# Optimization experiments

Measured on AMD Instinct MI355X. Metric: run time of the kernel, lower is better.

## Reference

```python
import jax, jax.numpy as jnp
import numpy as np

B, N, C = 4, 2048, 768
H = 12
D = C // H  # 64
HID = 4 * C  # 3072
EPS = 1e-5


def layer_norm(x, g, b):
    mu = jnp.mean(x, axis=-1, keepdims=True)
    var = jnp.mean(jnp.square(x - mu), axis=-1, keepdims=True)
    return (x - mu) * jax.lax.rsqrt(var + EPS) * g + b


def setup_inputs() -> dict:
    key = jax.random.key(0)
    ks = jax.random.split(key, 12)
    s = lambda fan_in: 1.0 / np.sqrt(fan_in)
    return {
        "x": jax.random.normal(ks[0], (B, N, C), jnp.float32),
        "ln1_g": jnp.ones((C,), jnp.float32),
        "ln1_b": jnp.zeros((C,), jnp.float32),
        "qkv_w": jax.random.normal(ks[1], (3 * C, C), jnp.float32) * s(C),
        "proj_w": jax.random.normal(ks[2], (C, C), jnp.float32) * s(C),
        "proj_b": jnp.zeros((C,), jnp.float32),
        "ln2_g": jnp.ones((C,), jnp.float32),
        "ln2_b": jnp.zeros((C,), jnp.float32),
        "fc1_w": jax.random.normal(ks[3], (HID, C), jnp.float32) * s(C),
        "fc1_b": jnp.zeros((HID,), jnp.float32),
        "fc2_w": jax.random.normal(ks[4], (C, HID), jnp.float32) * s(HID),
        "fc2_b": jnp.zeros((C,), jnp.float32),
    }


def reference(x, ln1_g, ln1_b, qkv_w, proj_w, proj_b, ln2_g, ln2_b, fc1_w, fc1_b, fc2_w, fc2_b):
    # ---- attention branch ----
    h = layer_norm(x, ln1_g, ln1_b)
    qkv = jnp.einsum('bnc,fc->bnf', h, qkv_w)            # [B,N,3C]
    qkv = qkv.reshape(B, N, 3, H, D)
    q, k, v = jnp.moveaxis(qkv, 2, 0)                     # each [B,N,H,D]
    q = jnp.transpose(q, (0, 2, 1, 3)) * (D ** -0.5)      # [B,H,N,D]
    k = jnp.transpose(k, (0, 2, 1, 3))
    v = jnp.transpose(v, (0, 2, 1, 3))
    attn = jax.nn.softmax(jnp.einsum('bhnd,bhmd->bhnm', q, k), axis=-1)
    o = jnp.einsum('bhnm,bhmd->bhnd', attn, v)            # [B,H,N,D]
    o = jnp.transpose(o, (0, 2, 1, 3)).reshape(B, N, C)
    o = jnp.einsum('bnc,oc->bno', o, proj_w) + proj_b
    x = x + o
    # ---- MLP branch ----
    h = layer_norm(x, ln2_g, ln2_b)
    h = jnp.einsum('bnc,hc->bnh', h, fc1_w) + fc1_b
    h = jax.nn.gelu(h, approximate=False)
    h = jnp.einsum('bnh,ch->bnc', h, fc2_w) + fc2_b
    return x + h
```

## Files before the change

kernel.cpp:

```cpp
#include <hip/hip_runtime.h>
#include <math.h>

typedef __bf16 bf16;
typedef __bf16 bf16x4 __attribute__((ext_vector_type(4)));
typedef __bf16 bf16x8 __attribute__((ext_vector_type(8)));
typedef float  f32x4  __attribute__((ext_vector_type(4)));

#define B_   4
#define N_   2048
#define C_   768
#define H_   12
#define T_   8192
#define HID_ 3072

typedef const __attribute__((address_space(1))) unsigned int* as1_u32;
typedef __attribute__((address_space(3))) unsigned int* as3_u32;
__device__ __forceinline__ void gl_lds16(const void* g, void* l) {
    __builtin_amdgcn_global_load_lds((as1_u32)g, (as3_u32)l, 16, 0, 0);
}

__global__ __launch_bounds__(256)
void ln_kernel(const float* __restrict__ inp, const float* __restrict__ g,
               const float* __restrict__ bsh, bf16* __restrict__ out)
{
    int wave = threadIdx.x >> 6, lane = threadIdx.x & 63;
    long long row = (long long)blockIdx.x * 4 + wave;
    const float* p = inp + row * C_;
    float v[12];
    #pragma unroll
    for (int i = 0; i < 12; i++) v[i] = p[i * 64 + lane];
    float s = 0.f, s2 = 0.f;
    #pragma unroll
    for (int i = 0; i < 12; i++) { s += v[i]; s2 += v[i] * v[i]; }
    #pragma unroll
    for (int m = 1; m < 64; m <<= 1) {
        s  += __shfl_xor(s,  m, 64);
        s2 += __shfl_xor(s2, m, 64);
    }
    float mu  = s  * (1.f / C_);
    float var = s2 * (1.f / C_) - mu * mu;
    float rs  = rsqrtf(var + 1e-5f);
    bf16* o = out + row * C_;
    #pragma unroll
    for (int i = 0; i < 12; i++) {
        int c = i * 64 + lane;
        o[c] = (bf16)(((v[i] - mu) * rs) * g[c] + bsh[c]);
    }
}

template<int MODE>
__global__ __launch_bounds__(256)
void gemm_bt(const bf16* __restrict__ A, const float* __restrict__ Bw,
             int M, int N, int K,
             const float* __restrict__ bias,
             const float* resid_f,
             void* out, bf16* out2)
{
    __shared__ bf16 At[128 * 32];
    __shared__ bf16 Bt[128 * 32];
    int tid  = threadIdx.x;
    int lane = tid & 63, wave = tid >> 6;
    int quad = lane >> 4, l15 = lane & 15;
    int bm = blockIdx.x, bn = blockIdx.y;
    int wm = wave >> 1, wn = wave & 1;

    f32x4 acc[4][4];
    f32x4 zero = {0.f, 0.f, 0.f, 0.f};
    #pragma unroll
    for (int mt = 0; mt < 4; mt++)
        #pragma unroll
        for (int nt = 0; nt < 4; nt++) acc[mt][nt] = zero;

    int arow = tid >> 2;
    int akof = (tid & 3) << 3;
    const bf16*  ag = A  + (size_t)(bm * 128 + arow) * K + akof;
    const float* bg = Bw + (size_t)(bn * 128 + arow) * K + akof;

    for (int k0 = 0; k0 < K; k0 += 32) {
        gl_lds16(ag,                    &At[tid * 8]);
        gl_lds16(ag + (size_t)64 * K,   &At[2048 + tid * 8]);
        f32x4 b0a = *(const f32x4*)(bg);
        f32x4 b0b = *(const f32x4*)(bg + 4);
        f32x4 b1a = *(const f32x4*)(bg + (size_t)64 * K);
        f32x4 b1b = *(const f32x4*)(bg + (size_t)64 * K + 4);
        bf16x8 b0, b1;
        #pragma unroll
        for (int j = 0; j < 4; j++) {
            b0[j] = (bf16)b0a[j]; b0[4 + j] = (bf16)b0b[j];
            b1[j] = (bf16)b1a[j]; b1[4 + j] = (bf16)b1b[j];
        }
        *(bf16x8*)(&Bt[tid * 8])        = b0;
        *(bf16x8*)(&Bt[2048 + tid * 8]) = b1;
        ag += 32; bg += 32;
        __syncthreads();

        bf16x8 af[4], bfr[4];
        #pragma unroll
        for (int mt = 0; mt < 4; mt++)
            af[mt] = *(const bf16x8*)(&At[(wm * 64 + mt * 16 + l15) * 32 + quad * 8]);
        #pragma unroll
        for (int nt = 0; nt < 4; nt++)
            bfr[nt] = *(const bf16x8*)(&Bt[(wn * 64 + nt * 16 + l15) * 32 + quad * 8]);
        #pragma unroll
        for (int mt = 0; mt < 4; mt++)
            #pragma unroll
            for (int nt = 0; nt < 4; nt++)
                acc[mt][nt] = __builtin_amdgcn_mfma_f32_16x16x32_bf16(
                    af[mt], bfr[nt], acc[mt][nt], 0, 0, 0);
        __syncthreads();
    }

    if (MODE == 3) {
        if (bn < 12) {
            #pragma unroll
            for (int nt = 0; nt < 4; nt++) {
                int col = bn * 128 + wn * 64 + nt * 16 + l15;
                #pragma unroll
                for (int mt = 0; mt < 4; mt++)
                    #pragma unroll
                    for (int r = 0; r < 4; r++) {
                        int row = bm * 128 + wm * 64 + mt * 16 + quad * 4 + r;
                        ((bf16*)out)[(size_t)row * 1536 + col] = (bf16)acc[mt][nt][r];
                    }
            }
        } else {
            int b = bm >> 4;
            #pragma unroll
            for (int nt = 0; nt < 4; nt++) {
                int vcol = bn * 128 - 1536 + wn * 64 + nt * 16 + l15;
                int h = vcol >> 6, d = vcol & 63;
                size_t rowbase = ((size_t)(b * H_ + h) * 64 + d) * N_;
                #pragma unroll
                for (int mt = 0; mt < 4; mt++) {
                    int n0 = (bm & 15) * 128 + wm * 64 + mt * 16 + quad * 4;
                    bf16x4 pv;
                    #pragma unroll
                    for (int r = 0; r < 4; r++) pv[r] = (bf16)acc[mt][nt][r];
                    *(bf16x4*)(&out2[rowbase + n0]) = pv;
                }
            }
        }
    } else {
        #pragma unroll
        for (int nt = 0; nt < 4; nt++) {
            int col = bn * 128 + wn * 64 + nt * 16 + l15;
            float bv = bias[col];
            #pragma unroll
            for (int mt = 0; mt < 4; mt++) {
                #pragma unroll
                for (int r = 0; r < 4; r++) {
                    int row = bm * 128 + wm * 64 + mt * 16 + quad * 4 + r;
                    size_t idx = (size_t)row * N + col;
                    float v = acc[mt][nt][r] + bv;
                    if (MODE == 1) {
                        ((float*)out)[idx] = v + resid_f[idx];
                    } else {
                        float ge = 0.5f * v * (1.f + erff(v * 0.70710678118f));
                        ((bf16*)out)[idx] = (bf16)ge;
                    }
                }
            }
        }
    }
}

__global__ __launch_bounds__(256)
void attn_kernel(const bf16* __restrict__ qk, const bf16* __restrict__ vt,
                 bf16* __restrict__ o)
{
    __shared__ bf16 Kt[2][64 * 64];
    __shared__ bf16 Vt[2][64 * 64];
    __shared__ bf16 Pt[4][2][16 * 64];

    int tid = threadIdx.x, lane = tid & 63, wave = tid >> 6;
    int quad = lane >> 4, l15 = lane & 15;
    int swz = (l15 & 7);
    int blk = blockIdx.x;
    int qb = blk & 15;
    int bh = blk >> 4;
    int b = bh / H_, h = bh % H_;

    const bf16* qbase = qk + (size_t)(b * N_) * 1536 + h * 64;
    const bf16* kbase = qbase + 768;
    const bf16* vtb   = vt + (size_t)(bh * 64) * N_;

    bf16x8 qf[2][2];
    #pragma unroll
    for (int qi = 0; qi < 2; qi++) {
        int q = qb * 128 + wave * 32 + qi * 16 + l15;
        const bf16* qp = qbase + (size_t)q * 1536 + quad * 8;
        qf[qi][0] = *(const bf16x8*)(qp);
        qf[qi][1] = *(const bf16x8*)(qp + 32);
    }

    int srow = tid >> 3, schk = tid & 7;
    int soA = srow * 64 + ((schk ^ (srow & 7)) << 3);
    int soB = (srow + 32) * 64 + ((schk ^ (srow & 7)) << 3);

    bf16x8 kr0, kr1, vr0, vr1;
    const bf16* kg0 = kbase + (size_t)srow * 1536 + schk * 8;
    const bf16* vg0 = vtb + (size_t)srow * N_ + schk * 8;

    {
        kr0 = *(const bf16x8*)(kg0);
        kr1 = *(const bf16x8*)(kg0 + (size_t)32 * 1536);
        vr0 = *(const bf16x8*)(vg0);
        vr1 = *(const bf16x8*)(vg0 + (size_t)32 * N_);
        *(bf16x8*)(&Kt[0][soA]) = kr0;  *(bf16x8*)(&Kt[0][soB]) = kr1;
        *(bf16x8*)(&Vt[0][soA]) = vr0;  *(bf16x8*)(&Vt[0][soB]) = vr1;
    }
    __syncthreads();

    f32x4 oacc[2][4];
    f32x4 zero = {0.f, 0.f, 0.f, 0.f};
    #pragma unroll
    for (int qi = 0; qi < 2; qi++)
        #pragma unroll
        for (int nt = 0; nt < 4; nt++) oacc[qi][nt] = zero;
    float mrun[2] = {-1e30f, -1e30f}, lrun[2] = {0.f, 0.f};

    for (int kt = 0; kt < 32; kt++) {
        int cur = kt & 1;
        if (kt < 31) {
            const bf16* kg = kg0 + (size_t)(kt + 1) * 64 * 1536;
            const bf16* vg = vg0 + (size_t)(kt + 1) * 64;
            kr0 = *(const bf16x8*)(kg);
            kr1 = *(const bf16x8*)(kg + (size_t)32 * 1536);
            vr0 = *(const bf16x8*)(vg);
            vr1 = *(const bf16x8*)(vg + (size_t)32 * N_);
        }
        const bf16* KtC = &Kt[cur][0];
        const bf16* VtC = &Vt[cur][0];

        #pragma unroll
        for (int qi = 0; qi < 2; qi++) {
            f32x4 s[4];
            #pragma unroll
            for (int nt = 0; nt < 4; nt++) {
                const bf16* krow = KtC + (nt * 16 + l15) * 64;
                bf16x8 ka0 = *(const bf16x8*)(krow + ((quad ^ swz) << 3));
                bf16x8 ka1 = *(const bf16x8*)(krow + (((4 + quad) ^ swz) << 3));
                f32x4 sv = zero;
                sv = __builtin_amdgcn_mfma_f32_16x16x32_bf16(ka0, qf[qi][0], sv, 0, 0, 0);
                sv = __builtin_amdgcn_mfma_f32_16x16x32_bf16(ka1, qf[qi][1], sv, 0, 0, 0);
                s[nt] = sv;
            }
            float mx = -1e30f;
            #pragma unroll
            for (int nt = 0; nt < 4; nt++)
                #pragma unroll
                for (int r = 0; r < 4; r++) mx = fmaxf(mx, s[nt][r]);
            mx = fmaxf(mx, __shfl_xor(mx, 16, 64));
            mx = fmaxf(mx, __shfl_xor(mx, 32, 64));
            float mnew = fmaxf(mrun[qi], mx * 0.125f);
            float al   = __expf(mrun[qi] - mnew);
            mrun[qi] = mnew;
            float ps = 0.f;
            #pragma unroll
            for (int nt = 0; nt < 4; nt++)
                #pragma unroll
                for (int r = 0; r < 4; r++) {
                    float pv = __expf(s[nt][r] * 0.125f - mnew);
                    s[nt][r] = pv;
                    ps += pv;
                }
            ps += __shfl_xor(ps, 16, 64);
            ps += __shfl_xor(ps, 32, 64);
            lrun[qi] = lrun[qi] * al + ps;
            #pragma unroll
            for (int nt = 0; nt < 4; nt++) oacc[qi][nt] *= al;
            bf16* pw = &Pt[wave][qi][0];
            #pragma unroll
            for (int nt = 0; nt < 4; nt++) {
                bf16x4 pk;
                #pragma unroll
                for (int r = 0; r < 4; r++) pk[r] = (bf16)s[nt][r];
                int ofs = l15 * 64 + (((nt * 2 + (quad >> 1)) ^ swz) << 3) + ((quad & 1) << 2);
                *(bf16x4*)(&pw[ofs]) = pk;
            }
        }

        #pragma unroll
        for (int kc = 0; kc < 2; kc++) {
            int pofs = l15 * 64 + (((kc * 4 + quad) ^ swz) << 3);
            bf16x8 pb0 = *(const bf16x8*)(&Pt[wave][0][pofs]);
            bf16x8 pb1 = *(const bf16x8*)(&Pt[wave][1][pofs]);
            #pragma unroll
            for (int nt = 0; nt < 4; nt++) {
                bf16x8 va = *(const bf16x8*)(VtC + (nt * 16 + l15) * 64 +
                                             (((kc * 4 + quad) ^ swz) << 3));
                oacc[0][nt] = __builtin_amdgcn_mfma_f32_16x16x32_bf16(va, pb0, oacc[0][nt], 0, 0, 0);
                oacc[1][nt] = __builtin_amdgcn_mfma_f32_16x16x32_bf16(va, pb1, oacc[1][nt], 0, 0, 0);
            }
        }

        if (kt < 31) {
            int nxt = cur ^ 1;
            *(bf16x8*)(&Kt[nxt][soA]) = kr0;  *(bf16x8*)(&Kt[nxt][soB]) = kr1;
            *(bf16x8*)(&Vt[nxt][soA]) = vr0;  *(bf16x8*)(&Vt[nxt][soB]) = vr1;
        }
        __syncthreads();
    }

    #pragma unroll
    for (int qi = 0; qi < 2; qi++) {
        int q = qb * 128 + wave * 32 + qi * 16 + l15;
        float inv = 1.f / lrun[qi];
        bf16* ob = o + (size_t)(b * N_ + q) * C_ + h * 64 + quad * 4;
        #pragma unroll
        for (int nt = 0; nt < 4; nt++) {
            bf16x4 pk;
            #pragma unroll
            for (int r = 0; r < 4; r++) pk[r] = (bf16)(oacc[qi][nt][r] * inv);
            *(bf16x4*)(&ob[nt * 16]) = pk;
        }
    }
}

extern "C" void kernel_launch(void* const* d_in, const int* in_sizes, int n_in,
                              void* d_out, int out_size, void* d_ws, size_t ws_size,
                              hipStream_t stream)
{
    const float* x      = (const float*)d_in[0];
    const float* ln1_g  = (const float*)d_in[1];
    const float* ln1_b  = (const float*)d_in[2];
    const float* qkv_w  = (const float*)d_in[3];
    const float* proj_w = (const float*)d_in[4];
    const float* proj_b = (const float*)d_in[5];
    const float* ln2_g  = (const float*)d_in[6];
    const float* ln2_b  = (const float*)d_in[7];
    const float* fc1_w  = (const float*)d_in[8];
    const float* fc1_b  = (const float*)d_in[9];
    const float* fc2_w  = (const float*)d_in[10];
    const float* fc2_b  = (const float*)d_in[11];
    float* out = (float*)d_out;

    char* ws = (char*)d_ws;
    bf16* QK = (bf16*)ws;
    bf16* VT = (bf16*)(ws + (size_t)T_ * 1536 * 2);
    bf16* G  = (bf16*)ws;
    bf16* R1 = (bf16*)(ws + (size_t)T_ * HID_ * 2);

    ln_kernel<<<T_ / 4, 256, 0, stream>>>(x, ln1_g, ln1_b, R1);
    gemm_bt<3><<<dim3(T_ / 128, 2304 / 128), 256, 0, stream>>>(
        R1, qkv_w, T_, 2304, C_, nullptr, nullptr, QK, VT);
    attn_kernel<<<48 * 16, 256, 0, stream>>>(QK, VT, R1);
    gemm_bt<1><<<dim3(T_ / 128, C_ / 128), 256, 0, stream>>>(
        R1, proj_w, T_, C_, C_, proj_b, x, out, nullptr);
    ln_kernel<<<T_ / 4, 256, 0, stream>>>(out, ln2_g, ln2_b, R1);
    gemm_bt<2><<<dim3(T_ / 128, HID_ / 128), 256, 0, stream>>>(
        R1, fc1_w, T_, HID_, C_, fc1_b, nullptr, G, nullptr);
    gemm_bt<1><<<dim3(T_ / 128, C_ / 128), 256, 0, stream>>>(
        G, fc2_w, T_, C_, HID_, fc2_b, out, out, nullptr);
}
```

Measured before the change: 555.2 us.

## Add swizzled LDS layout and double-buffered 128x64 GEMM for C-output projections

Applies an XOR swizzle to the LDS tile layout in the main GEMM to reduce bank conflicts on fragment reads. Adds a new gemm64 kernel with 128x64 tiles and double-buffered LDS for the proj and fc2 GEMMs (N=768). This doubles the block count on those narrow-output GEMMs for better CU occupancy and overlaps global loads with MFMA. The cost is reloading the A tiles more often, and the B tile is still converted from fp32 synchronously inside the loop.

```diff
diff --git a/kernel.cpp b/kernel.cpp
--- a/kernel.cpp
+++ b/kernel.cpp
@@ -53,7 +53,6 @@
 void gemm_bt(const bf16* __restrict__ A, const float* __restrict__ Bw,
              int M, int N, int K,
              const float* __restrict__ bias,
-             const float* resid_f,
              void* out, bf16* out2)
 {
     __shared__ bf16 At[128 * 32];
@@ -63,6 +62,7 @@
     int quad = lane >> 4, l15 = lane & 15;
     int bm = blockIdx.x, bn = blockIdx.y;
     int wm = wave >> 1, wn = wave & 1;
+    int swz = (l15 >> 1) & 3;
 
     f32x4 acc[4][4];
     f32x4 zero = {0.f, 0.f, 0.f, 0.f};
@@ -72,9 +72,9 @@
         for (int nt = 0; nt < 4; nt++) acc[mt][nt] = zero;
 
     int arow = tid >> 2;
-    int akof = (tid & 3) << 3;
-    const bf16*  ag = A  + (size_t)(bm * 128 + arow) * K + akof;
-    const float* bg = Bw + (size_t)(bn * 128 + arow) * K + akof;
+    int aq   = (tid & 3) ^ ((arow >> 1) & 3);
+    const bf16*  ag = A  + (size_t)(bm * 128 + arow) * K + aq * 8;
+    const float* bg = Bw + (size_t)(bn * 128 + arow) * K + aq * 8;
 
     for (int k0 = 0; k0 < K; k0 += 32) {
         gl_lds16(ag,                    &At[tid * 8]);
@@ -97,10 +97,10 @@
         bf16x8 af[4], bfr[4];
         #pragma unroll
         for (int mt = 0; mt < 4; mt++)
-            af[mt] = *(const bf16x8*)(&At[(wm * 64 + mt * 16 + l15) * 32 + quad * 8]);
+            af[mt] = *(const bf16x8*)(&At[wm * 2048 + (mt * 16 + l15) * 32 + ((quad ^ swz) << 3)]);
         #pragma unroll
         for (int nt = 0; nt < 4; nt++)
-            bfr[nt] = *(const bf16x8*)(&Bt[(wn * 64 + nt * 16 + l15) * 32 + quad * 8]);
+            bfr[nt] = *(const bf16x8*)(&Bt[wn * 2048 + (nt * 16 + l15) * 32 + ((quad ^ swz) << 3)]);
         #pragma unroll
         for (int mt = 0; mt < 4; mt++)
             #pragma unroll
@@ -152,13 +152,94 @@
                     int row = bm * 128 + wm * 64 + mt * 16 + quad * 4 + r;
                     size_t idx = (size_t)row * N + col;
                     float v = acc[mt][nt][r] + bv;
-                    if (MODE == 1) {
-                        ((float*)out)[idx] = v + resid_f[idx];
-                    } else {
-                        float ge = 0.5f * v * (1.f + erff(v * 0.70710678118f));
-                        ((bf16*)out)[idx] = (bf16)ge;
-                    }
+                    float ge = 0.5f * v * (1.f + erff(v * 0.70710678118f));
+                    ((bf16*)out)[idx] = (bf16)ge;
                 }
+            }
+        }
+    }
+}
+
+__global__ __launch_bounds__(256)
+void gemm64(const bf16* __restrict__ A, const float* __restrict__ Bw,
+            int K, const float* __restrict__ bias,
+            const float* resid_f, float* out)
+{
+    __shared__ bf16 At[2][128 * 32];
+    __shared__ bf16 Bt[2][64 * 32];
+    int tid  = threadIdx.x;
+    int lane = tid & 63, wave = tid >> 6;
+    int quad = lane >> 4, l15 = lane & 15;
+    int bm = blockIdx.x, bn = blockIdx.y;
+    int wm = wave >> 1, wn = wave & 1;
+    int swz = (l15 >> 1) & 3;
+
+    f32x4 acc[4][2];
+    f32x4 zero = {0.f, 0.f, 0.f, 0.f};
+    #pragma unroll
+    for (int mt = 0; mt < 4; mt++)
+        #pragma unroll
+        for (int nt = 0; nt < 2; nt++) acc[mt][nt] = zero;
+
+    int arow = tid >> 2;
+    int aq   = (tid & 3) ^ ((arow >> 1) & 3);
+    const bf16*  ag = A  + (size_t)(bm * 128 + arow) * K + aq * 8;
+    const float* bg = Bw + (size_t)(bn * 64  + arow) * K + aq * 8;
+
+    {
+        gl_lds16(ag,                  &At[0][tid * 8]);
+        gl_lds16(ag + (size_t)64 * K, &At[0][2048 + tid * 8]);
+        f32x4 ba = *(const f32x4*)(bg);
+        f32x4 bb = *(const f32x4*)(bg + 4);
+        bf16x8 b0;
+        #pragma unroll
+        for (int j = 0; j < 4; j++) { b0[j] = (bf16)ba[j]; b0[4 + j] = (bf16)bb[j]; }
+        *(bf16x8*)(&Bt[0][tid * 8]) = b0;
+    }
+    __syncthreads();
+
+    int nk = K >> 5;
+    for (int kt = 0; kt < nk; kt++) {
+        int cur = kt & 1, nxt = cur ^ 1;
+        if (kt + 1 < nk) {
+            const bf16*  agn = ag + (size_t)(kt + 1) * 32;
+            const float* bgn = bg + (size_t)(kt + 1) * 32;
+            gl_lds16(agn,                  &At[nxt][tid * 8]);
+            gl_lds16(agn + (size_t)64 * K, &At[nxt][2048 + tid * 8]);
+            f32x4 ba = *(const f32x4*)(bgn);
+            f32x4 bb = *(const f32x4*)(bgn + 4);
+            bf16x8 b0;
+            #pragma unroll
+            for (int j = 0; j < 4; j++) { b0[j] = (bf16)ba[j]; b0[4 + j] = (bf16)bb[j]; }
+            *(bf16x8*)(&Bt[nxt][tid * 8]) = b0;
+        }
+        bf16x8 af[4], bfr[2];
+        #pragma unroll
+        for (int mt = 0; mt < 4; mt++)
+            af[mt] = *(const bf16x8*)(&At[cur][wm * 2048 + (mt * 16 + l15) * 32 + ((quad ^ swz) << 3)]);
+        #pragma unroll
+        for (int nt = 0; nt < 2; nt++)
+            bfr[nt] = *(const bf16x8*)(&Bt[cur][(wn * 32 + nt * 16 + l15) * 32 + ((quad ^ swz) << 3)]);
+        #pragma unroll
+        for (int mt = 0; mt < 4; mt++)
+            #pragma unroll
+            for (int nt = 0; nt < 2; nt++)
+                acc[mt][nt] = __builtin_amdgcn_mfma_f32_16x16x32_bf16(
+                    af[mt], bfr[nt], acc[mt][nt], 0, 0, 0);
+        __syncthreads();
+    }
+
+    #pragma unroll
+    for (int nt = 0; nt < 2; nt++) {
+        int col = bn * 64 + wn * 32 + nt * 16 + l15;
+        float bv = bias[col];
+        #pragma unroll
+        for (int mt = 0; mt < 4; mt++) {
+            #pragma unroll
+            for (int r = 0; r < 4; r++) {
+                int row = bm * 128 + wm * 64 + mt * 16 + quad * 4 + r;
+                size_t idx = (size_t)row * C_ + col;
+                out[idx] = acc[mt][nt][r] + bv + resid_f[idx];
             }
         }
     }
@@ -343,13 +424,13 @@
 
     ln_kernel<<<T_ / 4, 256, 0, stream>>>(x, ln1_g, ln1_b, R1);
     gemm_bt<3><<<dim3(T_ / 128, 2304 / 128), 256, 0, stream>>>(
-        R1, qkv_w, T_, 2304, C_, nullptr, nullptr, QK, VT);
+        R1, qkv_w, T_, 2304, C_, nullptr, QK, VT);
     attn_kernel<<<48 * 16, 256, 0, stream>>>(QK, VT, R1);
-    gemm_bt<1><<<dim3(T_ / 128, C_ / 128), 256, 0, stream>>>(
-        R1, proj_w, T_, C_, C_, proj_b, x, out, nullptr);
+    gemm64<<<dim3(T_ / 128, C_ / 64), 256, 0, stream>>>(
+        R1, proj_w, C_, proj_b, x, out);
     ln_kernel<<<T_ / 4, 256, 0, stream>>>(out, ln2_g, ln2_b, R1);
     gemm_bt<2><<<dim3(T_ / 128, HID_ / 128), 256, 0, stream>>>(
-        R1, fc1_w, T_, HID_, C_, fc1_b, nullptr, G, nullptr);
-    gemm_bt<1><<<dim3(T_ / 128, C_ / 128), 256, 0, stream>>>(
-        G, fc2_w, T_, C_, HID_, fc2_b, out, out, nullptr);
-}
+        R1, fc1_w, T_, HID_, C_, fc1_b, G, nullptr);
+    gemm64<<<dim3(T_ / 128, C_ / 64), 256, 0, stream>>>(
+        G, fc2_w, HID_, fc2_b, out, out);
+}
```

Result: faster. 527.0 us (-5.1%).
